# Kernel optimization log

Hardware: AMD Instinct MI355X
Metric: run time of the kernel (lower is better)

The kernel has to match this reference:

```python
import jax, jax.numpy as jnp
import numpy as np

Q_MAX = 127.0  # 2**(8-1) - 1
EPS = 1e-08


def quantize_activation(x):
    # per-tensor symmetric int8 quant with STE
    scale = jnp.maximum(jnp.max(jnp.abs(x)) / Q_MAX, EPS)
    x_scaled = x / scale
    rounded = jnp.clip(jnp.round(x_scaled), -Q_MAX, Q_MAX)
    # STE: forward = rounded, backward = identity w.r.t. x_scaled
    q = x_scaled + jax.lax.stop_gradient(rounded - x_scaled)
    return q, jax.lax.stop_gradient(scale)


def ternarize_weight(W):
    scale = jnp.mean(jnp.abs(W)) + EPS
    W_norm = W / scale
    rounded = jnp.clip(jnp.round(W_norm), -1.0, 1.0)
    # STE: forward = rounded, backward = identity w.r.t. W
    tW = W + jax.lax.stop_gradient(rounded - W)
    return tW, jax.lax.stop_gradient(scale)


def setup_inputs() -> dict:
    key = jax.random.key(0)
    kx, kw = jax.random.split(key)
    in_features, out_features = 4096, 11008
    x = jax.random.normal(kx, (4, 2048, in_features), dtype=jnp.float32)
    # kaiming_uniform_(a=sqrt(5)) -> U(-bound, bound), bound = sqrt(6/((1+a^2)*fan_in)) = 1/sqrt(fan_in)
    bound = 1.0 / np.sqrt(in_features)
    W = jax.random.uniform(kw, (out_features, in_features), dtype=jnp.float32,
                           minval=-bound, maxval=bound)
    return {"x": x, "W": W}


def reference(x, W):
    qx, act_scale = quantize_activation(x)
    tW, w_scale = ternarize_weight(W)
    # F.linear: x @ W.T ; [b, s, in] x [out, in] -> [b, s, out]
    out = jnp.einsum('bsi,oi->bso', qx, tW)
    return out * (w_scale * act_scale)
```

## Files before the change

kernel.cpp:

```cpp
#include <hip/hip_runtime.h>
#include <cstdint>

typedef int i32x4 __attribute__((ext_vector_type(4)));
typedef int i32x16 __attribute__((ext_vector_type(16)));

#define M_DIM 8192
#define N_DIM 11008
#define K_DIM 4096
#define NTILES 64
#define DEPTH 4

#define WS_AMAX_OFF   0
#define WS_WSUM_OFF   4096
#define WS_SCALES_OFF 12288
#define WS_QX_OFF     16384
#define WS_TW_OFF     (16384 + 33554432)

__device__ __forceinline__ void gload_lds16(const void* g, void* l) {
  __builtin_amdgcn_global_load_lds(
      (const __attribute__((address_space(1))) unsigned int*)g,
      (__attribute__((address_space(3))) unsigned int*)l, 16, 0, 0);
}


__global__ void reduce_amax(const float* __restrict__ x, float* __restrict__ partial, int n4) {
  const float4* xv = (const float4*)x;
  float m = 0.f;
  for (long i = (long)blockIdx.x * blockDim.x + threadIdx.x; i < n4;
       i += (long)gridDim.x * blockDim.x) {
    float4 v = xv[i];
    m = fmaxf(m, fmaxf(fmaxf(fabsf(v.x), fabsf(v.y)), fmaxf(fabsf(v.z), fabsf(v.w))));
  }
  __shared__ float sm[256];
  sm[threadIdx.x] = m;
  __syncthreads();
  for (int s = 128; s > 0; s >>= 1) {
    if (threadIdx.x < s) sm[threadIdx.x] = fmaxf(sm[threadIdx.x], sm[threadIdx.x + s]);
    __syncthreads();
  }
  if (threadIdx.x == 0) partial[blockIdx.x] = sm[0];
}

__global__ void reduce_wsum(const float* __restrict__ w, double* __restrict__ partial, int n4) {
  const float4* wv = (const float4*)w;
  double acc = 0.0;
  for (long i = (long)blockIdx.x * blockDim.x + threadIdx.x; i < n4;
       i += (long)gridDim.x * blockDim.x) {
    float4 v = wv[i];
    acc += (double)fabsf(v.x) + (double)fabsf(v.y) + (double)fabsf(v.z) + (double)fabsf(v.w);
  }
  __shared__ double sd[256];
  sd[threadIdx.x] = acc;
  __syncthreads();
  for (int s = 128; s > 0; s >>= 1) {
    if (threadIdx.x < s) sd[threadIdx.x] += sd[threadIdx.x + s];
    __syncthreads();
  }
  if (threadIdx.x == 0) partial[blockIdx.x] = sd[0];
}

__global__ void finalize_scales(const float* __restrict__ amax_p,
                                const double* __restrict__ wsum_p,
                                float* __restrict__ scales) {
  __shared__ float sm[1024];
  __shared__ double sd[1024];
  const int t = threadIdx.x;
  sm[t] = amax_p[t];
  sd[t] = wsum_p[t];
  __syncthreads();
  for (int s = 512; s > 0; s >>= 1) {
    if (t < s) {
      sm[t] = fmaxf(sm[t], sm[t + s]);
      sd[t] += sd[t + s];
    }
    __syncthreads();
  }
  if (t == 0) {
    float act_scale = fmaxf(sm[0] / 127.0f, 1e-8f);
    float w_scale = (float)(sd[0] / (double)((long long)N_DIM * K_DIM)) + 1e-8f;
    scales[0] = act_scale;
    scales[1] = w_scale;
    scales[2] = act_scale * w_scale;
  }
}


__device__ __forceinline__ int quant_clip(float v, float s, float lim) {
  float r = rintf(v / s);
  r = fminf(fmaxf(r, -lim), lim);
  return (int)r;
}

__global__ void quant_x(const float* __restrict__ x, const float* __restrict__ scales,
                        int8_t* __restrict__ q) {
  const float s = scales[0];
  const long i = (long)blockIdx.x * blockDim.x + threadIdx.x;
  const float4* xv = (const float4*)x + (i << 2);
  i32x4 pk;
#pragma unroll
  for (int j = 0; j < 4; ++j) {
    float4 v = xv[j];
    int b0 = quant_clip(v.x, s, 127.f);
    int b1 = quant_clip(v.y, s, 127.f);
    int b2 = quant_clip(v.z, s, 127.f);
    int b3 = quant_clip(v.w, s, 127.f);
    pk[j] = (b0 & 255) | ((b1 & 255) << 8) | ((b2 & 255) << 16) | (b3 << 24);
  }
  *((i32x4*)q + i) = pk;
}

__global__ void tern_w(const float* __restrict__ w, const float* __restrict__ scales,
                       int8_t* __restrict__ q) {
  const float s = scales[1];
  const long i = (long)blockIdx.x * blockDim.x + threadIdx.x;
  const float4* wv = (const float4*)w + (i << 2);
  i32x4 pk;
#pragma unroll
  for (int j = 0; j < 4; ++j) {
    float4 v = wv[j];
    int b0 = quant_clip(v.x, s, 1.f);
    int b1 = quant_clip(v.y, s, 1.f);
    int b2 = quant_clip(v.z, s, 1.f);
    int b3 = quant_clip(v.w, s, 1.f);
    pk[j] = (b0 & 255) | ((b1 & 255) << 8) | ((b2 & 255) << 16) | (b3 << 24);
  }
  *((i32x4*)q + i) = pk;
}


__global__ __launch_bounds__(512, 2) void gemm_i8(const int8_t* __restrict__ qx,
                                                  const int8_t* __restrict__ tw,
                                                  const float* __restrict__ scales,
                                                  float* __restrict__ out) {
  __shared__ __align__(16) int8_t lds[DEPTH][32768];

  const int tid = threadIdx.x;
  const int l = tid & 63;
  const int w = tid >> 6;
  const int lane31 = l & 31;
  const int khalf = l >> 5;

  const int bid = blockIdx.x;
  const int xcd = bid & 7;
  const int local = bid >> 3;
  const int ni = local >> 2;
  const int mi = (xcd << 2) + (local & 3);
  const long row0 = (long)mi << 8;
  const long col0 = (long)ni << 8;

  const int srow = ((l >> 3) << 1) + ((l >> 2) & 1);
  const int schk = ((l & 3) ^ ((l >> 3) & 3)) << 4;
  const int8_t* pA = qx + (row0 + 32 * w + srow) * (long)K_DIM + schk;
  const int8_t* pB = tw + (col0 + 32 * w + srow) * (long)K_DIM + schk;
  const int ldsA = w << 11;
  const int ldsB = 16384 + (w << 11);

  auto stage = [&](int d, int kt) {
    const long cb = (long)kt << 6;
    gload_lds16(pA + cb, lds[d] + ldsA);
    gload_lds16(pA + cb + 16 * (long)K_DIM, lds[d] + ldsA + 1024);
    gload_lds16(pB + cb, lds[d] + ldsB);
    gload_lds16(pB + cb + 16 * (long)K_DIM, lds[d] + ldsB + 1024);
  };

  const int rbl = ((lane31 >> 1) << 7) + ((lane31 & 1) << 6);
  const int x4 = (lane31 >> 1) & 3;
  int cOffR[4];
#pragma unroll
  for (int c = 0; c < 4; ++c) cOffR[c] = ((c ^ x4) << 4);
  const int aBase = ((w >> 2) << 13) + rbl;
  const int bBase = 16384 + ((w & 3) << 12) + rbl;

  i32x16 acc[4][2];
#pragma unroll
  for (int mf = 0; mf < 4; ++mf)
#pragma unroll
    for (int nf = 0; nf < 2; ++nf)
#pragma unroll
      for (int e = 0; e < 16; ++e) acc[mf][nf][e] = 0;

  stage(0, 0);
  stage(1, 1);
  stage(2, 2);

#pragma unroll 4
  for (int t = 0; t < NTILES; ++t) {
    asm volatile("s_waitcnt vmcnt(8)" ::: "memory");
    asm volatile("s_waitcnt lgkmcnt(0)" ::: "memory");
    __builtin_amdgcn_s_barrier();
    asm volatile("" ::: "memory");

    const int kt3 = (t + 3 < NTILES) ? t + 3 : NTILES - 1;
    stage((t + 3) & 3, kt3);

    const int8_t* buf = lds[t & 3];

    i32x4 a0[4], a1[4], b0[2], b1[2];
#pragma unroll
    for (int mf = 0; mf < 4; ++mf) {
      a0[mf] = *(const i32x4*)(buf + aBase + mf * 2048 + cOffR[khalf]);
      a1[mf] = *(const i32x4*)(buf + aBase + mf * 2048 + cOffR[2 + khalf]);
    }
#pragma unroll
    for (int nf = 0; nf < 2; ++nf) {
      b0[nf] = *(const i32x4*)(buf + bBase + nf * 2048 + cOffR[khalf]);
      b1[nf] = *(const i32x4*)(buf + bBase + nf * 2048 + cOffR[2 + khalf]);
    }

    __builtin_amdgcn_s_setprio(1);
#pragma unroll
    for (int mf = 0; mf < 4; ++mf) {
      acc[mf][0] = __builtin_amdgcn_mfma_i32_32x32x32_i8(a0[mf], b0[0], acc[mf][0], 0, 0, 0);
      acc[mf][1] = __builtin_amdgcn_mfma_i32_32x32x32_i8(a0[mf], b0[1], acc[mf][1], 0, 0, 0);
    }
#pragma unroll
    for (int mf = 0; mf < 4; ++mf) {
      acc[mf][0] = __builtin_amdgcn_mfma_i32_32x32x32_i8(a1[mf], b1[0], acc[mf][0], 0, 0, 0);
      acc[mf][1] = __builtin_amdgcn_mfma_i32_32x32x32_i8(a1[mf], b1[1], acc[mf][1], 0, 0, 0);
    }
    __builtin_amdgcn_s_setprio(0);
  }

  const float osc = scales[2];
  const int rbase = khalf << 2;
#pragma unroll
  for (int mf = 0; mf < 4; ++mf)
#pragma unroll
    for (int nf = 0; nf < 2; ++nf)
#pragma unroll
      for (int reg = 0; reg < 16; ++reg) {
        int rr = (w >> 2) * 128 + mf * 32 + rbase + (reg & 3) + ((reg >> 2) << 3);
        int cc = (w & 3) * 64 + nf * 32 + lane31;
        out[(row0 + rr) * (long)N_DIM + (col0 + cc)] = (float)acc[mf][nf][reg] * osc;
      }
}


extern "C" void kernel_launch(void* const* d_in, const int* in_sizes, int n_in,
                              void* d_out, int out_size, void* d_ws, size_t ws_size,
                              hipStream_t stream) {
  const float* x = (const float*)d_in[0];
  const float* W = (const float*)d_in[1];
  float* out = (float*)d_out;

  char* ws = (char*)d_ws;
  float*  amax_p = (float*)(ws + WS_AMAX_OFF);
  double* wsum_p = (double*)(ws + WS_WSUM_OFF);
  float*  scales = (float*)(ws + WS_SCALES_OFF);
  int8_t* qx = (int8_t*)(ws + WS_QX_OFF);
  int8_t* tw = (int8_t*)(ws + WS_TW_OFF);

  reduce_amax<<<1024, 256, 0, stream>>>(x, amax_p, (M_DIM * (long)K_DIM) / 4);
  reduce_wsum<<<1024, 256, 0, stream>>>(W, wsum_p, (N_DIM * (long)K_DIM) / 4);
  finalize_scales<<<1, 1024, 0, stream>>>(amax_p, wsum_p, scales);
  quant_x<<<(M_DIM * (long)K_DIM) / 16 / 256, 256, 0, stream>>>(x, scales, qx);
  tern_w<<<(N_DIM * (long)K_DIM) / 16 / 256, 256, 0, stream>>>(W, scales, tw);

  const int grid = (M_DIM / 256) * (N_DIM / 256);
  gemm_i8<<<grid, 512, 0, stream>>>(qx, tw, scales, out);
}
```

Before: 552.2 us.

## Prefetch next-tile LDS fragments into registers for the second wave group

Waves 4-7 now read the next tile's A/B fragments from LDS right after issuing their MFMAs for the current tile. This double-buffers fragments in registers so their LDS reads overlap the matrix work. Waves 0-3 keep the old read-then-compute order, so the two groups stagger their LDS and MFMA phases. The global-load wait is tightened to vmcnt(4) so the next tile is resident before the barrier, and the explicit lgkmcnt wait is dropped. The cost is a shallower effective global prefetch depth and extra fragment registers, which may add register pressure at two blocks per CU.

```diff
diff --git a/kernel.cpp b/kernel.cpp
--- a/kernel.cpp
+++ b/kernel.cpp
@@ -179,46 +179,64 @@
 #pragma unroll
       for (int e = 0; e < 16; ++e) acc[mf][nf][e] = 0;
 
+  i32x4 fa0[4], fa1[4], fb0[2], fb1[2];
+
+  auto read_frags = [&](const int8_t* buf) {
+#pragma unroll
+    for (int mf = 0; mf < 4; ++mf)
+      fa0[mf] = *(const i32x4*)(buf + aBase + mf * 2048 + cOffR[khalf]);
+#pragma unroll
+    for (int nf = 0; nf < 2; ++nf)
+      fb0[nf] = *(const i32x4*)(buf + bBase + nf * 2048 + cOffR[khalf]);
+#pragma unroll
+    for (int mf = 0; mf < 4; ++mf)
+      fa1[mf] = *(const i32x4*)(buf + aBase + mf * 2048 + cOffR[2 + khalf]);
+#pragma unroll
+    for (int nf = 0; nf < 2; ++nf)
+      fb1[nf] = *(const i32x4*)(buf + bBase + nf * 2048 + cOffR[2 + khalf]);
+  };
+
+  auto mfma_all = [&]() {
+    __builtin_amdgcn_s_setprio(1);
+#pragma unroll
+    for (int mf = 0; mf < 4; ++mf) {
+      acc[mf][0] = __builtin_amdgcn_mfma_i32_32x32x32_i8(fa0[mf], fb0[0], acc[mf][0], 0, 0, 0);
+      acc[mf][1] = __builtin_amdgcn_mfma_i32_32x32x32_i8(fa0[mf], fb0[1], acc[mf][1], 0, 0, 0);
+    }
+#pragma unroll
+    for (int mf = 0; mf < 4; ++mf) {
+      acc[mf][0] = __builtin_amdgcn_mfma_i32_32x32x32_i8(fa1[mf], fb1[0], acc[mf][0], 0, 0, 0);
+      acc[mf][1] = __builtin_amdgcn_mfma_i32_32x32x32_i8(fa1[mf], fb1[1], acc[mf][1], 0, 0, 0);
+    }
+    __builtin_amdgcn_s_setprio(0);
+  };
+
+  const bool g1 = (w >= 4);
+
   stage(0, 0);
   stage(1, 1);
   stage(2, 2);
 
 #pragma unroll 4
   for (int t = 0; t < NTILES; ++t) {
-    asm volatile("s_waitcnt vmcnt(8)" ::: "memory");
-    asm volatile("s_waitcnt lgkmcnt(0)" ::: "memory");
+    asm volatile("s_waitcnt vmcnt(4)" ::: "memory");
     __builtin_amdgcn_s_barrier();
     asm volatile("" ::: "memory");
 
     const int kt3 = (t + 3 < NTILES) ? t + 3 : NTILES - 1;
     stage((t + 3) & 3, kt3);
 
-    const int8_t* buf = lds[t & 3];
-
-    i32x4 a0[4], a1[4], b0[2], b1[2];
-#pragma unroll
-    for (int mf = 0; mf < 4; ++mf) {
-      a0[mf] = *(const i32x4*)(buf + aBase + mf * 2048 + cOffR[khalf]);
-      a1[mf] = *(const i32x4*)(buf + aBase + mf * 2048 + cOffR[2 + khalf]);
-    }
-#pragma unroll
-    for (int nf = 0; nf < 2; ++nf) {
-      b0[nf] = *(const i32x4*)(buf + bBase + nf * 2048 + cOffR[khalf]);
-      b1[nf] = *(const i32x4*)(buf + bBase + nf * 2048 + cOffR[2 + khalf]);
-    }
-
-    __builtin_amdgcn_s_setprio(1);
-#pragma unroll
-    for (int mf = 0; mf < 4; ++mf) {
-      acc[mf][0] = __builtin_amdgcn_mfma_i32_32x32x32_i8(a0[mf], b0[0], acc[mf][0], 0, 0, 0);
-      acc[mf][1] = __builtin_amdgcn_mfma_i32_32x32x32_i8(a0[mf], b0[1], acc[mf][1], 0, 0, 0);
-    }
-#pragma unroll
-    for (int mf = 0; mf < 4; ++mf) {
-      acc[mf][0] = __builtin_amdgcn_mfma_i32_32x32x32_i8(a1[mf], b1[0], acc[mf][0], 0, 0, 0);
-      acc[mf][1] = __builtin_amdgcn_mfma_i32_32x32x32_i8(a1[mf], b1[1], acc[mf][1], 0, 0, 0);
-    }
-    __builtin_amdgcn_s_setprio(0);
+    const int8_t* bufc = lds[t & 3];
+    const int8_t* bufn = lds[(t + 1) & 3];
+
+    if (!g1) {
+      read_frags(bufc);
+      mfma_all();
+    } else {
+      if (t == 0) read_frags(bufc);
+      mfma_all();
+      if (t + 1 < NTILES) read_frags(bufn);
+    }
   }
 
   const float osc = scales[2];
```

Measured after the change: 1.087 ms. 1.97x slower.

## Pre-pack quantized operands into MFMA fragment layout; load B directly to registers

Applied to the files above, without the earlier changes.

The quantization kernels now write qx and tW in a packed layout where each 1KB block is already in the 32x32x32 MFMA fragment order, using an LDS transpose inside the quant kernel. The GEMM then streams A into a double-buffered LDS ring with contiguous global-to-LDS loads and reads B fragments straight from global memory into registers, prefetching one tile ahead. This removes swizzled LDS addressing and halves LDS use per block. In exchange the pipeline depth drops from four stages to two, a full __syncthreads is added every tile, and B is read from global without LDS sharing across waves.

```diff
diff --git a/kernel.cpp b/kernel.cpp
--- a/kernel.cpp
+++ b/kernel.cpp
@@ -7,8 +7,8 @@
 #define M_DIM 8192
 #define N_DIM 11008
 #define K_DIM 4096
+#define K32   (K_DIM / 32)
 #define NTILES 64
-#define DEPTH 4
 
 #define WS_AMAX_OFF   0
 #define WS_WSUM_OFF   4096
@@ -91,48 +91,42 @@
   return (int)r;
 }
 
-__global__ void quant_x(const float* __restrict__ x, const float* __restrict__ scales,
-                        int8_t* __restrict__ q) {
-  const float s = scales[0];
-  const long i = (long)blockIdx.x * blockDim.x + threadIdx.x;
-  const float4* xv = (const float4*)x + (i << 2);
+template <int LIM_IS_W>
+__global__ void quant_pack(const float* __restrict__ src, const float* __restrict__ scales,
+                           int8_t* __restrict__ qp) {
+  __shared__ __align__(16) int8_t buf[32 * 144];
+  const float s = scales[LIM_IS_W ? 1 : 0];
+  const float lim = LIM_IS_W ? 1.f : 127.f;
+  const int br = blockIdx.x >> 5;
+  const int bk = blockIdx.x & 31;
+  const int t = threadIdx.x;
+
+  const int row = t >> 3, kc = (t & 7) << 4;
+  const float4* sp = (const float4*)(src + ((long)(br * 32 + row)) * K_DIM + bk * 128 + kc);
   i32x4 pk;
 #pragma unroll
   for (int j = 0; j < 4; ++j) {
-    float4 v = xv[j];
-    int b0 = quant_clip(v.x, s, 127.f);
-    int b1 = quant_clip(v.y, s, 127.f);
-    int b2 = quant_clip(v.z, s, 127.f);
-    int b3 = quant_clip(v.w, s, 127.f);
+    float4 v = sp[j];
+    int b0 = quant_clip(v.x, s, lim);
+    int b1 = quant_clip(v.y, s, lim);
+    int b2 = quant_clip(v.z, s, lim);
+    int b3 = quant_clip(v.w, s, lim);
     pk[j] = (b0 & 255) | ((b1 & 255) << 8) | ((b2 & 255) << 16) | (b3 << 24);
   }
-  *((i32x4*)q + i) = pk;
-}
-
-__global__ void tern_w(const float* __restrict__ w, const float* __restrict__ scales,
-                       int8_t* __restrict__ q) {
-  const float s = scales[1];
-  const long i = (long)blockIdx.x * blockDim.x + threadIdx.x;
-  const float4* wv = (const float4*)w + (i << 2);
-  i32x4 pk;
-#pragma unroll
-  for (int j = 0; j < 4; ++j) {
-    float4 v = wv[j];
-    int b0 = quant_clip(v.x, s, 1.f);
-    int b1 = quant_clip(v.y, s, 1.f);
-    int b2 = quant_clip(v.z, s, 1.f);
-    int b3 = quant_clip(v.w, s, 1.f);
-    pk[j] = (b0 & 255) | ((b1 & 255) << 8) | ((b2 & 255) << 16) | (b3 << 24);
-  }
-  *((i32x4*)q + i) = pk;
-}
-
-
-__global__ __launch_bounds__(512, 2) void gemm_i8(const int8_t* __restrict__ qx,
-                                                  const int8_t* __restrict__ tw,
+  *(i32x4*)(buf + row * 144 + kc) = pk;
+  __syncthreads();
+
+  const int g = t >> 6, l = t & 63;
+  i32x4 fr = *(const i32x4*)(buf + (l & 31) * 144 + g * 32 + ((l >> 5) << 4));
+  *((i32x4*)(qp + ((long)br * K32 + bk * 4 + g) * 1024) + l) = fr;
+}
+
+
+__global__ __launch_bounds__(512, 2) void gemm_i8(const int8_t* __restrict__ qxp,
+                                                  const int8_t* __restrict__ twp,
                                                   const float* __restrict__ scales,
                                                   float* __restrict__ out) {
-  __shared__ __align__(16) int8_t lds[DEPTH][32768];
+  __shared__ __align__(16) int8_t lds[2][16384];
 
   const int tid = threadIdx.x;
   const int l = tid & 63;
@@ -148,28 +142,23 @@
   const long row0 = (long)mi << 8;
   const long col0 = (long)ni << 8;
 
-  const int srow = ((l >> 3) << 1) + ((l >> 2) & 1);
-  const int schk = ((l & 3) ^ ((l >> 3) & 3)) << 4;
-  const int8_t* pA = qx + (row0 + 32 * w + srow) * (long)K_DIM + schk;
-  const int8_t* pB = tw + (col0 + 32 * w + srow) * (long)K_DIM + schk;
-  const int ldsA = w << 11;
-  const int ldsB = 16384 + (w << 11);
-
-  auto stage = [&](int d, int kt) {
-    const long cb = (long)kt << 6;
-    gload_lds16(pA + cb, lds[d] + ldsA);
-    gload_lds16(pA + cb + 16 * (long)K_DIM, lds[d] + ldsA + 1024);
-    gload_lds16(pB + cb, lds[d] + ldsB);
-    gload_lds16(pB + cb + 16 * (long)K_DIM, lds[d] + ldsB + 1024);
+  const int8_t* aSrc = qxp + ((long)(mi * 8 + w) * K32) * 1024 + l * 16;
+  auto stageA = [&](int slot, int kt) {
+    gload_lds16(aSrc + (long)(2 * kt) * 1024, &lds[slot][w * 2048]);
+    gload_lds16(aSrc + (long)(2 * kt + 1) * 1024, &lds[slot][w * 2048 + 1024]);
   };
 
-  const int rbl = ((lane31 >> 1) << 7) + ((lane31 & 1) << 6);
-  const int x4 = (lane31 >> 1) & 3;
-  int cOffR[4];
-#pragma unroll
-  for (int c = 0; c < 4; ++c) cOffR[c] = ((c ^ x4) << 4);
-  const int aBase = ((w >> 2) << 13) + rbl;
-  const int bBase = 16384 + ((w & 3) << 12) + rbl;
+  const int8_t* bSrc0 = twp + ((long)(ni * 8 + (w & 3) * 2) * K32) * 1024 + l * 16;
+  const int8_t* bSrc1 = bSrc0 + (long)K32 * 1024;
+  auto loadB = [&](i32x4 (&dst)[4], int kt) {
+    const long o = (long)(2 * kt) * 1024;
+    dst[0] = *(const i32x4*)(bSrc0 + o);
+    dst[1] = *(const i32x4*)(bSrc0 + o + 1024);
+    dst[2] = *(const i32x4*)(bSrc1 + o);
+    dst[3] = *(const i32x4*)(bSrc1 + o + 1024);
+  };
+
+  const int aRd = ((w >> 2) * 8) * 1024 + l * 16;
 
   i32x16 acc[4][2];
 #pragma unroll
@@ -179,46 +168,38 @@
 #pragma unroll
       for (int e = 0; e < 16; ++e) acc[mf][nf][e] = 0;
 
-  stage(0, 0);
-  stage(1, 1);
-  stage(2, 2);
-
-#pragma unroll 4
-  for (int t = 0; t < NTILES; ++t) {
-    asm volatile("s_waitcnt vmcnt(8)" ::: "memory");
-    asm volatile("s_waitcnt lgkmcnt(0)" ::: "memory");
-    __builtin_amdgcn_s_barrier();
-    asm volatile("" ::: "memory");
-
-    const int kt3 = (t + 3 < NTILES) ? t + 3 : NTILES - 1;
-    stage((t + 3) & 3, kt3);
-
-    const int8_t* buf = lds[t & 3];
-
-    i32x4 a0[4], a1[4], b0[2], b1[2];
+  auto body = [&](int t, i32x4 (&bcur)[4], i32x4 (&bnext)[4]) {
+    const int cur = t & 1;
+    const int ktn = (t + 1 < NTILES) ? t + 1 : NTILES - 1;
+    stageA(cur ^ 1, ktn);
+    loadB(bnext, ktn);
+    const int8_t* buf = lds[cur];
+    i32x4 af[4][2];
+#pragma unroll
+    for (int mf = 0; mf < 4; ++mf)
+#pragma unroll
+      for (int sl = 0; sl < 2; ++sl)
+        af[mf][sl] = *(const i32x4*)(buf + aRd + (mf * 2 + sl) * 1024);
+    __builtin_amdgcn_s_setprio(1);
 #pragma unroll
     for (int mf = 0; mf < 4; ++mf) {
-      a0[mf] = *(const i32x4*)(buf + aBase + mf * 2048 + cOffR[khalf]);
-      a1[mf] = *(const i32x4*)(buf + aBase + mf * 2048 + cOffR[2 + khalf]);
-    }
-#pragma unroll
-    for (int nf = 0; nf < 2; ++nf) {
-      b0[nf] = *(const i32x4*)(buf + bBase + nf * 2048 + cOffR[khalf]);
-      b1[nf] = *(const i32x4*)(buf + bBase + nf * 2048 + cOffR[2 + khalf]);
-    }
-
-    __builtin_amdgcn_s_setprio(1);
-#pragma unroll
-    for (int mf = 0; mf < 4; ++mf) {
-      acc[mf][0] = __builtin_amdgcn_mfma_i32_32x32x32_i8(a0[mf], b0[0], acc[mf][0], 0, 0, 0);
-      acc[mf][1] = __builtin_amdgcn_mfma_i32_32x32x32_i8(a0[mf], b0[1], acc[mf][1], 0, 0, 0);
-    }
-#pragma unroll
-    for (int mf = 0; mf < 4; ++mf) {
-      acc[mf][0] = __builtin_amdgcn_mfma_i32_32x32x32_i8(a1[mf], b1[0], acc[mf][0], 0, 0, 0);
-      acc[mf][1] = __builtin_amdgcn_mfma_i32_32x32x32_i8(a1[mf], b1[1], acc[mf][1], 0, 0, 0);
+      acc[mf][0] = __builtin_amdgcn_mfma_i32_32x32x32_i8(af[mf][0], bcur[0], acc[mf][0], 0, 0, 0);
+      acc[mf][1] = __builtin_amdgcn_mfma_i32_32x32x32_i8(af[mf][0], bcur[2], acc[mf][1], 0, 0, 0);
+      acc[mf][0] = __builtin_amdgcn_mfma_i32_32x32x32_i8(af[mf][1], bcur[1], acc[mf][0], 0, 0, 0);
+      acc[mf][1] = __builtin_amdgcn_mfma_i32_32x32x32_i8(af[mf][1], bcur[3], acc[mf][1], 0, 0, 0);
     }
     __builtin_amdgcn_s_setprio(0);
+    __syncthreads();
+  };
+
+  i32x4 bEv[4], bOd[4];
+  stageA(0, 0);
+  loadB(bEv, 0);
+  __syncthreads();
+
+  for (int tp = 0; tp < NTILES / 2; ++tp) {
+    body(2 * tp, bEv, bOd);
+    body(2 * tp + 1, bOd, bEv);
   }
 
   const float osc = scales[2];
@@ -247,15 +228,15 @@
   float*  amax_p = (float*)(ws + WS_AMAX_OFF);
   double* wsum_p = (double*)(ws + WS_WSUM_OFF);
   float*  scales = (float*)(ws + WS_SCALES_OFF);
-  int8_t* qx = (int8_t*)(ws + WS_QX_OFF);
-  int8_t* tw = (int8_t*)(ws + WS_TW_OFF);
+  int8_t* qxp = (int8_t*)(ws + WS_QX_OFF);
+  int8_t* twp = (int8_t*)(ws + WS_TW_OFF);
 
   reduce_amax<<<1024, 256, 0, stream>>>(x, amax_p, (M_DIM * (long)K_DIM) / 4);
   reduce_wsum<<<1024, 256, 0, stream>>>(W, wsum_p, (N_DIM * (long)K_DIM) / 4);
   finalize_scales<<<1, 1024, 0, stream>>>(amax_p, wsum_p, scales);
-  quant_x<<<(M_DIM * (long)K_DIM) / 16 / 256, 256, 0, stream>>>(x, scales, qx);
-  tern_w<<<(N_DIM * (long)K_DIM) / 16 / 256, 256, 0, stream>>>(W, scales, tw);
+  quant_pack<0><<<(M_DIM / 32) * 32, 256, 0, stream>>>(x, scales, qxp);
+  quant_pack<1><<<(N_DIM / 32) * 32, 256, 0, stream>>>(W, scales, twp);
 
   const int grid = (M_DIM / 256) * (N_DIM / 256);
-  gemm_i8<<<grid, 512, 0, stream>>>(qx, tw, scales, out);
-}
+  gemm_i8<<<grid, 512, 0, stream>>>(qxp, twp, scales, out);
+}
```

Result: no change. 549.3 us (-0.5%).
